# Optimization experiments

Hardware: AMD Instinct MI355X
Metric: run time of the kernel (lower is better)

Reference implementation:

```python
import jax, jax.numpy as jnp
import numpy as np

N_NODES = 50000
N_EDGES = 800000
IN_DIM, HID_DIM, OUT_DIM = 64, 128, 32


def _mpnn_layer(x, src, dst, W, b):
    # message: linear on gathered source features (x_j), then mean-scatter to dst
    msg = x[src] @ W + b                      # [E, out]
    agg = jax.ops.segment_sum(msg, dst, num_segments=N_NODES)
    deg = jax.ops.segment_sum(jnp.ones((msg.shape[0],), msg.dtype), dst,
                              num_segments=N_NODES)
    return agg / jnp.maximum(deg, 1.0)[:, None]  # mean; isolated nodes -> 0


def setup_inputs() -> dict:
    key = jax.random.key(0)
    ks = jax.random.split(key, 8)
    x = jax.random.normal(ks[0], (N_NODES, IN_DIM), dtype=jnp.float32)
    edge_index = jax.random.randint(ks[1], (2, N_EDGES), 0, N_NODES, dtype=jnp.int64)
    W1 = jax.random.normal(ks[2], (IN_DIM, HID_DIM), dtype=jnp.float32) * 0.1
    b1 = jax.random.normal(ks[3], (HID_DIM,), dtype=jnp.float32) * 0.1
    W2 = jax.random.normal(ks[4], (HID_DIM, HID_DIM), dtype=jnp.float32) * 0.1
    b2 = jax.random.normal(ks[5], (HID_DIM,), dtype=jnp.float32) * 0.1
    Wout = jax.random.normal(ks[6], (HID_DIM, OUT_DIM), dtype=jnp.float32) * 0.1
    bout = jax.random.normal(ks[7], (OUT_DIM,), dtype=jnp.float32) * 0.1
    return {"x": x, "edge_index": edge_index, "W1": W1, "b1": b1,
            "W2": W2, "b2": b2, "Wout": Wout, "bout": bout}


def reference(x, edge_index, W1, b1, W2, b2, Wout, bout):
    src, dst = edge_index[0], edge_index[1]  # PyG flow: source_to_target
    h = jax.nn.relu(_mpnn_layer(x, src, dst, W1, b1))
    h = jax.nn.relu(_mpnn_layer(h, src, dst, W2, b2))
    return h @ Wout + bout
```

## Files before the change

### kernel.cpp

```cpp
#include <hip/hip_runtime.h>
#include <hip/hip_bf16.h>

#define N_NODES 50000
#define N_EDGES 800000
#define IN_DIM  64
#define HID_DIM 128
#define OUT_DIM 32
#define ELLW    64

#define NRANGE   8
#define RNG      (N_NODES / NRANGE)
#define ELL_NJ   ((N_EDGES + 255) / 256)

#define CAST_BLKS 3125
#define PW1_BLKS  32
#define PW2_BLKS  64
#define PWO_BLKS  16
#define ZERO_BLKS 49

typedef short bh8_t  __attribute__((ext_vector_type(8)));
typedef float fx4_t  __attribute__((ext_vector_type(4)));

__device__ inline float bflo(unsigned int u) {
    union { unsigned int i; float f; } c; c.i = u << 16; return c.f;
}
__device__ inline float bfhi(unsigned int u) {
    union { unsigned int i; float f; } c; c.i = u & 0xffff0000u; return c.f;
}
__device__ inline unsigned short f2bf(float f) {
    union { float f; unsigned int i; } c; c.f = f;
    unsigned int u = c.i;
    u += 0x7fffu + ((u >> 16) & 1u);
    return (unsigned short)(u >> 16);
}
__device__ inline unsigned int pack2(float a, float b) {
    return (unsigned int)f2bf(a) | ((unsigned int)f2bf(b) << 16);
}
__device__ inline void acc_u4(float* a, uint4 u) {
    a[0] += bflo(u.x); a[1] += bfhi(u.x);
    a[2] += bflo(u.y); a[3] += bfhi(u.y);
    a[4] += bflo(u.z); a[5] += bfhi(u.z);
    a[6] += bflo(u.w); a[7] += bfhi(u.w);
}

template <int K, int M>
__device__ inline void packw_one(const float* __restrict__ W,
                                 unsigned short* __restrict__ Wp, int f) {
    const int k = f / M, m = f % M;
    Wp[((k >> 3) * M + m) * 8 + (k & 7)] = f2bf(W[f]);
}

__global__ void k_prep(const float* __restrict__ x, unsigned short* __restrict__ xb,
                       const float* __restrict__ W1, unsigned short* __restrict__ wp1,
                       const float* __restrict__ W2, unsigned short* __restrict__ wp2,
                       const float* __restrict__ Wout, unsigned short* __restrict__ wpo,
                       int* __restrict__ cnt) {
    const int bid = blockIdx.x;
    if (bid < CAST_BLKS) {
        const int i = bid * 256 + threadIdx.x;
        float4 v = reinterpret_cast<const float4*>(x)[i];
        ushort4 o;
        o.x = f2bf(v.x); o.y = f2bf(v.y); o.z = f2bf(v.z); o.w = f2bf(v.w);
        reinterpret_cast<ushort4*>(xb)[i] = o;
    } else if (bid < CAST_BLKS + PW1_BLKS) {
        packw_one<IN_DIM, HID_DIM>(W1, wp1, (bid - CAST_BLKS) * 256 + threadIdx.x);
    } else if (bid < CAST_BLKS + PW1_BLKS + PW2_BLKS) {
        packw_one<HID_DIM, HID_DIM>(W2, wp2, (bid - CAST_BLKS - PW1_BLKS) * 256 + threadIdx.x);
    } else if (bid < CAST_BLKS + PW1_BLKS + PW2_BLKS + PWO_BLKS) {
        packw_one<HID_DIM, OUT_DIM>(Wout, wpo,
                                    (bid - CAST_BLKS - PW1_BLKS - PW2_BLKS) * 256 + threadIdx.x);
    } else {
        const int zb = bid - (CAST_BLKS + PW1_BLKS + PW2_BLKS + PWO_BLKS);
#pragma unroll
        for (int k2 = 0; k2 < 4; ++k2) {
            const int i = zb * 1024 + k2 * 256 + threadIdx.x;
            if (i < N_NODES) cnt[i] = 0;
        }
    }
}

__global__ __launch_bounds__(256) void k_ell(const int* __restrict__ src,
                                             const int* __restrict__ dst,
                                             int* __restrict__ cnt,
                                             int* __restrict__ ell) {
    const int r  = blockIdx.x & (NRANGE - 1);
    const int j  = blockIdx.x >> 3;
    const int lo = r * RNG;
    const int e  = j * 256 + threadIdx.x;
    const int d  = dst[e];
    if ((unsigned)(d - lo) < (unsigned)RNG) {
        const int p = atomicAdd(&cnt[d], 1);
        if (p < ELLW) ell[(size_t)d * ELLW + p] = src[e];
    }
}

__global__ __launch_bounds__(256) void k_ag1(const unsigned short* __restrict__ xb,
                                             const int* __restrict__ ell,
                                             const int* __restrict__ cnt,
                                             const unsigned short* __restrict__ wp1g,
                                             const float* __restrict__ b1,
                                             unsigned short* __restrict__ h1b) {
    __shared__ unsigned short wp1s[IN_DIM * HID_DIM];
    __shared__ unsigned short m1s[64][72];
    const int tid = threadIdx.x;
#pragma unroll
    for (int f = tid; f < IN_DIM * HID_DIM / 8; f += 256)
        reinterpret_cast<uint4*>(wp1s)[f] = reinterpret_cast<const uint4*>(wp1g)[f];

    const int nloc = tid >> 2, l4 = tid & 3;
    const int node = blockIdx.x * 64 + nloc;
    int c = 0;
    if (node < N_NODES) c = min(cnt[node], ELLW);
    const float inv = (c > 0) ? 1.0f / (float)c : 0.0f;
    const int* er = ell + (size_t)node * ELLW;
    const unsigned short* xbb = xb + l4 * 16;

    float a0[16], a1[16];
#pragma unroll
    for (int v = 0; v < 16; ++v) { a0[v] = 0.f; a1[v] = 0.f; }

    int j = 0;
    for (; j + 4 <= c; j += 4) {
        const int4 e4 = *reinterpret_cast<const int4*>(er + j);
        const unsigned short* r0 = xbb + (size_t)e4.x * IN_DIM;
        const unsigned short* r1 = xbb + (size_t)e4.y * IN_DIM;
        const unsigned short* r2 = xbb + (size_t)e4.z * IN_DIM;
        const unsigned short* r3 = xbb + (size_t)e4.w * IN_DIM;
        uint4 u00 = reinterpret_cast<const uint4*>(r0)[0];
        uint4 u01 = reinterpret_cast<const uint4*>(r0)[1];
        uint4 u10 = reinterpret_cast<const uint4*>(r1)[0];
        uint4 u11 = reinterpret_cast<const uint4*>(r1)[1];
        uint4 u20 = reinterpret_cast<const uint4*>(r2)[0];
        uint4 u21 = reinterpret_cast<const uint4*>(r2)[1];
        uint4 u30 = reinterpret_cast<const uint4*>(r3)[0];
        uint4 u31 = reinterpret_cast<const uint4*>(r3)[1];
        acc_u4(a0, u00); acc_u4(a0 + 8, u01);
        acc_u4(a1, u10); acc_u4(a1 + 8, u11);
        acc_u4(a0, u20); acc_u4(a0 + 8, u21);
        acc_u4(a1, u30); acc_u4(a1 + 8, u31);
    }
    for (; j < c; ++j) {
        const unsigned short* r0 = xbb + (size_t)er[j] * IN_DIM;
        uint4 u00 = reinterpret_cast<const uint4*>(r0)[0];
        uint4 u01 = reinterpret_cast<const uint4*>(r0)[1];
        acc_u4(a0, u00); acc_u4(a0 + 8, u01);
    }

    unsigned int* mw = reinterpret_cast<unsigned int*>(&m1s[nloc][l4 * 16]);
#pragma unroll
    for (int i = 0; i < 8; ++i)
        mw[i] = pack2((a0[2 * i] + a1[2 * i]) * inv,
                      (a0[2 * i + 1] + a1[2 * i + 1]) * inv);
    __syncthreads();

    const int w  = tid >> 6;
    const int l  = tid & 63;
    const int lr = l & 15;
    const int lg = l >> 4;

    fx4_t acc[8];
#pragma unroll
    for (int ct = 0; ct < 8; ++ct) acc[ct] = (fx4_t){0.f, 0.f, 0.f, 0.f};

#pragma unroll
    for (int kc = 0; kc < IN_DIM; kc += 32) {
        const bh8_t af = *reinterpret_cast<const bh8_t*>(&m1s[w * 16 + lr][kc + lg * 8]);
#pragma unroll
        for (int ct = 0; ct < 8; ++ct) {
            const bh8_t bf = *reinterpret_cast<const bh8_t*>(
                &wp1s[(((kc >> 3) + lg) * HID_DIM + ct * 16 + lr) * 8]);
            acc[ct] = __builtin_amdgcn_mfma_f32_16x16x32_bf16(af, bf, acc[ct], 0, 0, 0);
        }
    }

    const int orow0 = blockIdx.x * 64 + w * 16 + lg * 4;
    bool on[4];
#pragma unroll
    for (int r = 0; r < 4; ++r)
        on[r] = (orow0 + r < N_NODES) && (cnt[orow0 + r] > 0);

#pragma unroll
    for (int ct = 0; ct < 8; ++ct) {
        const int m = ct * 16 + lr;
        const float bm = b1[m];
#pragma unroll
        for (int r = 0; r < 4; ++r) {
            const int n = orow0 + r;
            if (n < N_NODES) {
                float v = on[r] ? fmaxf(acc[ct][r] + bm, 0.f) : 0.f;
                h1b[(size_t)n * HID_DIM + m] = f2bf(v);
            }
        }
    }
}

__global__ __launch_bounds__(256) void k_agg2(const unsigned short* __restrict__ Xb,
                                              const int* __restrict__ ell,
                                              const int* __restrict__ cnt,
                                              unsigned short* __restrict__ Mb) {
    const int gid  = threadIdx.x >> 4;
    const int lane = threadIdx.x & 15;
    const int node = blockIdx.x * 16 + gid;
    const int c = min(cnt[node], ELLW);
    const float r = (c > 0) ? 1.0f / (float)c : 0.0f;
    const int* er = ell + (size_t)node * ELLW;
    const unsigned short* base = Xb + lane * 8;

    float a0[8], a1[8];
#pragma unroll
    for (int v = 0; v < 8; ++v) { a0[v] = 0.f; a1[v] = 0.f; }

    int j = 0;
    for (; j + 8 <= c; j += 8) {
        const int4 e03 = *reinterpret_cast<const int4*>(er + j);
        const int4 e47 = *reinterpret_cast<const int4*>(er + j + 4);
        uint4 u0 = *reinterpret_cast<const uint4*>(base + (size_t)e03.x * HID_DIM);
        uint4 u1 = *reinterpret_cast<const uint4*>(base + (size_t)e03.y * HID_DIM);
        uint4 u2 = *reinterpret_cast<const uint4*>(base + (size_t)e03.z * HID_DIM);
        uint4 u3 = *reinterpret_cast<const uint4*>(base + (size_t)e03.w * HID_DIM);
        uint4 u4 = *reinterpret_cast<const uint4*>(base + (size_t)e47.x * HID_DIM);
        uint4 u5 = *reinterpret_cast<const uint4*>(base + (size_t)e47.y * HID_DIM);
        uint4 u6 = *reinterpret_cast<const uint4*>(base + (size_t)e47.z * HID_DIM);
        uint4 u7 = *reinterpret_cast<const uint4*>(base + (size_t)e47.w * HID_DIM);
        acc_u4(a0, u0); acc_u4(a1, u1); acc_u4(a0, u2); acc_u4(a1, u3);
        acc_u4(a0, u4); acc_u4(a1, u5); acc_u4(a0, u6); acc_u4(a1, u7);
    }
    for (; j + 4 <= c; j += 4) {
        const int4 e4 = *reinterpret_cast<const int4*>(er + j);
        uint4 u0 = *reinterpret_cast<const uint4*>(base + (size_t)e4.x * HID_DIM);
        uint4 u1 = *reinterpret_cast<const uint4*>(base + (size_t)e4.y * HID_DIM);
        uint4 u2 = *reinterpret_cast<const uint4*>(base + (size_t)e4.z * HID_DIM);
        uint4 u3 = *reinterpret_cast<const uint4*>(base + (size_t)e4.w * HID_DIM);
        acc_u4(a0, u0); acc_u4(a1, u1); acc_u4(a0, u2); acc_u4(a1, u3);
    }
    for (; j < c; ++j) {
        uint4 u = *reinterpret_cast<const uint4*>(base + (size_t)er[j] * HID_DIM);
        acc_u4(a0, u);
    }

    uint4 o;
    o.x = pack2((a0[0] + a1[0]) * r, (a0[1] + a1[1]) * r);
    o.y = pack2((a0[2] + a1[2]) * r, (a0[3] + a1[3]) * r);
    o.z = pack2((a0[4] + a1[4]) * r, (a0[5] + a1[5]) * r);
    o.w = pack2((a0[6] + a1[6]) * r, (a0[7] + a1[7]) * r);
    *reinterpret_cast<uint4*>(Mb + (size_t)node * HID_DIM + lane * 8) = o;
}

#define H2S (HID_DIM + 8)
__global__ __launch_bounds__(256) void k_mgemm23(const unsigned short* __restrict__ A,
                                                 const unsigned short* __restrict__ Wp2g,
                                                 const unsigned short* __restrict__ Wpog,
                                                 const float* __restrict__ b2,
                                                 const float* __restrict__ bout,
                                                 const int* __restrict__ cnt,
                                                 float* __restrict__ out) {
    __shared__ unsigned short Wp2s[HID_DIM * HID_DIM];
    __shared__ unsigned short Wpos[HID_DIM * OUT_DIM];
    __shared__ unsigned short h2s[64 * H2S];
    const int tid = threadIdx.x;
#pragma unroll
    for (int f = tid; f < HID_DIM * HID_DIM / 8; f += 256)
        reinterpret_cast<uint4*>(Wp2s)[f] = reinterpret_cast<const uint4*>(Wp2g)[f];
#pragma unroll
    for (int f = tid; f < HID_DIM * OUT_DIM / 8; f += 256)
        reinterpret_cast<uint4*>(Wpos)[f] = reinterpret_cast<const uint4*>(Wpog)[f];
    __syncthreads();

    const int w  = tid >> 6;
    const int l  = tid & 63;
    const int lr = l & 15;
    const int lg = l >> 4;
    const int row = blockIdx.x * 64 + w * 16 + lr;
    const bool rok = row < N_NODES;
    const unsigned short* Arow = A + (size_t)row * HID_DIM;

    fx4_t acc[8];
#pragma unroll
    for (int ct = 0; ct < 8; ++ct) acc[ct] = (fx4_t){0.f, 0.f, 0.f, 0.f};

#pragma unroll
    for (int kc = 0; kc < HID_DIM; kc += 32) {
        bh8_t af = {};
        if (rok) af = *reinterpret_cast<const bh8_t*>(Arow + kc + lg * 8);
#pragma unroll
        for (int ct = 0; ct < 8; ++ct) {
            const bh8_t bf = *reinterpret_cast<const bh8_t*>(
                &Wp2s[(((kc >> 3) + lg) * HID_DIM + ct * 16 + lr) * 8]);
            acc[ct] = __builtin_amdgcn_mfma_f32_16x16x32_bf16(af, bf, acc[ct], 0, 0, 0);
        }
    }

    const int lrow0 = w * 16 + lg * 4;
    const int orow0 = blockIdx.x * 64 + lrow0;
    bool on[4];
#pragma unroll
    for (int r = 0; r < 4; ++r)
        on[r] = (orow0 + r < N_NODES) && (cnt[orow0 + r] > 0);

#pragma unroll
    for (int ct = 0; ct < 8; ++ct) {
        const int m = ct * 16 + lr;
        const float bm = b2[m];
#pragma unroll
        for (int r = 0; r < 4; ++r) {
            float v = on[r] ? fmaxf(acc[ct][r] + bm, 0.f) : 0.f;
            h2s[(lrow0 + r) * H2S + m] = f2bf(v);
        }
    }
    __syncthreads();

    fx4_t acc2[2];
#pragma unroll
    for (int ct = 0; ct < 2; ++ct) acc2[ct] = (fx4_t){0.f, 0.f, 0.f, 0.f};

#pragma unroll
    for (int kc = 0; kc < HID_DIM; kc += 32) {
        const bh8_t af = *reinterpret_cast<const bh8_t*>(
            &h2s[(w * 16 + lr) * H2S + kc + lg * 8]);
#pragma unroll
        for (int ct = 0; ct < 2; ++ct) {
            const bh8_t bf = *reinterpret_cast<const bh8_t*>(
                &Wpos[(((kc >> 3) + lg) * OUT_DIM + ct * 16 + lr) * 8]);
            acc2[ct] = __builtin_amdgcn_mfma_f32_16x16x32_bf16(af, bf, acc2[ct], 0, 0, 0);
        }
    }

#pragma unroll
    for (int ct = 0; ct < 2; ++ct) {
        const int m = ct * 16 + lr;
        const float bm = bout[m];
#pragma unroll
        for (int r = 0; r < 4; ++r) {
            const int n = orow0 + r;
            if (n < N_NODES)
                out[(size_t)n * OUT_DIM + m] = acc2[ct][r] + bm;
        }
    }
}

extern "C" void kernel_launch(void* const* d_in, const int* in_sizes, int n_in,
                              void* d_out, int out_size, void* d_ws, size_t ws_size,
                              hipStream_t stream) {
    const float* x    = (const float*)d_in[0];
    const int*   ei   = (const int*)d_in[1];
    const float* W1   = (const float*)d_in[2];
    const float* b1   = (const float*)d_in[3];
    const float* W2   = (const float*)d_in[4];
    const float* b2   = (const float*)d_in[5];
    const float* Wout = (const float*)d_in[6];
    const float* bout = (const float*)d_in[7];
    float* out = (float*)d_out;

    const int* src = ei;
    const int* dst = ei + N_EDGES;

    char* ws = (char*)d_ws;
    int*            cnt = (int*)(ws + 0);
    int*            ell = (int*)(ws + 200000);
    unsigned short* xb  = (unsigned short*)(ws + 13000000);
    unsigned short* h1b = (unsigned short*)(ws + 19400000);
    unsigned short* m2b = (unsigned short*)(ws + 32200000);
    unsigned short* wp1 = (unsigned short*)(ws + 45000000);
    unsigned short* wp2 = (unsigned short*)(ws + 45016384);
    unsigned short* wpo = (unsigned short*)(ws + 45049152);

    const int GB = (N_NODES + 63) / 64;
    const int AB = N_NODES / 16;

    k_prep<<<CAST_BLKS + PW1_BLKS + PW2_BLKS + PWO_BLKS + ZERO_BLKS, 256, 0, stream>>>(
        x, xb, W1, wp1, W2, wp2, Wout, wpo, cnt);
    k_ell<<<ELL_NJ * NRANGE, 256, 0, stream>>>(src, dst, cnt, ell);

    k_ag1<<<GB, 256, 0, stream>>>(xb, ell, cnt, wp1, b1, h1b);

    k_agg2<<<AB, 256, 0, stream>>>(h1b, ell, cnt, m2b);

    k_mgemm23<<<GB, 256, 0, stream>>>(m2b, wp2, wpo, b2, bout, cnt, out);
}
```

Measured before the change: 137.2 us.

## Merge ELL build with prep, split layer-1 aggregation from GEMM, zero counts via memset

Fuses the ELL construction and the cast/weight-pack work into one launch, zeroing the degree counters with hipMemsetAsync beforehand. Layer-1 aggregation moves to a standalone kernel with 16 lanes per node and 8-byte gathers plus deeper unrolling, which writes a bf16 mean buffer. A separate MFMA GEMM kernel then reads that buffer. This aims for more parallel, latency-tolerant gathers and fewer serialized small kernels, at the cost of an extra intermediate round trip through global memory and one more launch.

```diff
diff --git a/kernel.cpp b/kernel.cpp
--- a/kernel.cpp
+++ b/kernel.cpp
@@ -10,13 +10,13 @@
 
 #define NRANGE   8
 #define RNG      (N_NODES / NRANGE)
-#define ELL_NJ   ((N_EDGES + 255) / 256)
+#define ELL_BLKS 25000
 
 #define CAST_BLKS 3125
 #define PW1_BLKS  32
 #define PW2_BLKS  64
 #define PWO_BLKS  16
-#define ZERO_BLKS 49
+#define PREP_BLKS (CAST_BLKS + PW1_BLKS + PW2_BLKS + PWO_BLKS)
 
 typedef short bh8_t  __attribute__((ext_vector_type(8)));
 typedef float fx4_t  __attribute__((ext_vector_type(4)));
@@ -36,6 +36,10 @@
 __device__ inline unsigned int pack2(float a, float b) {
     return (unsigned int)f2bf(a) | ((unsigned int)f2bf(b) << 16);
 }
+__device__ inline void acc_u2(float* a, uint2 u) {
+    a[0] += bflo(u.x); a[1] += bfhi(u.x);
+    a[2] += bflo(u.y); a[3] += bfhi(u.y);
+}
 __device__ inline void acc_u4(float* a, uint4 u) {
     a[0] += bflo(u.x); a[1] += bfhi(u.x);
     a[2] += bflo(u.y); a[3] += bfhi(u.y);
@@ -50,113 +54,117 @@
     Wp[((k >> 3) * M + m) * 8 + (k & 7)] = f2bf(W[f]);
 }
 
-__global__ void k_prep(const float* __restrict__ x, unsigned short* __restrict__ xb,
-                       const float* __restrict__ W1, unsigned short* __restrict__ wp1,
-                       const float* __restrict__ W2, unsigned short* __restrict__ wp2,
-                       const float* __restrict__ Wout, unsigned short* __restrict__ wpo,
-                       int* __restrict__ cnt) {
+__global__ __launch_bounds__(256) void k_pe(const int* __restrict__ src,
+                                            const int* __restrict__ dst,
+                                            int* __restrict__ cnt,
+                                            int* __restrict__ ell,
+                                            const float* __restrict__ x,
+                                            unsigned short* __restrict__ xb,
+                                            const float* __restrict__ W1,
+                                            unsigned short* __restrict__ wp1,
+                                            const float* __restrict__ W2,
+                                            unsigned short* __restrict__ wp2,
+                                            const float* __restrict__ Wout,
+                                            unsigned short* __restrict__ wpo) {
     const int bid = blockIdx.x;
-    if (bid < CAST_BLKS) {
-        const int i = bid * 256 + threadIdx.x;
+    if (bid < ELL_BLKS) {
+        const int r  = bid & (NRANGE - 1);
+        const int j  = bid >> 3;
+        const int lo = r * RNG;
+        const int e  = j * 256 + threadIdx.x;
+        const int d  = dst[e];
+        if ((unsigned)(d - lo) < (unsigned)RNG) {
+            const int p = atomicAdd(&cnt[d], 1);
+            if (p < ELLW) ell[(size_t)d * ELLW + p] = src[e];
+        }
+        return;
+    }
+    const int pb = bid - ELL_BLKS;
+    if (pb < CAST_BLKS) {
+        const int i = pb * 256 + threadIdx.x;
         float4 v = reinterpret_cast<const float4*>(x)[i];
         ushort4 o;
         o.x = f2bf(v.x); o.y = f2bf(v.y); o.z = f2bf(v.z); o.w = f2bf(v.w);
         reinterpret_cast<ushort4*>(xb)[i] = o;
-    } else if (bid < CAST_BLKS + PW1_BLKS) {
-        packw_one<IN_DIM, HID_DIM>(W1, wp1, (bid - CAST_BLKS) * 256 + threadIdx.x);
-    } else if (bid < CAST_BLKS + PW1_BLKS + PW2_BLKS) {
-        packw_one<HID_DIM, HID_DIM>(W2, wp2, (bid - CAST_BLKS - PW1_BLKS) * 256 + threadIdx.x);
-    } else if (bid < CAST_BLKS + PW1_BLKS + PW2_BLKS + PWO_BLKS) {
+    } else if (pb < CAST_BLKS + PW1_BLKS) {
+        packw_one<IN_DIM, HID_DIM>(W1, wp1, (pb - CAST_BLKS) * 256 + threadIdx.x);
+    } else if (pb < CAST_BLKS + PW1_BLKS + PW2_BLKS) {
+        packw_one<HID_DIM, HID_DIM>(W2, wp2, (pb - CAST_BLKS - PW1_BLKS) * 256 + threadIdx.x);
+    } else {
         packw_one<HID_DIM, OUT_DIM>(Wout, wpo,
-                                    (bid - CAST_BLKS - PW1_BLKS - PW2_BLKS) * 256 + threadIdx.x);
-    } else {
-        const int zb = bid - (CAST_BLKS + PW1_BLKS + PW2_BLKS + PWO_BLKS);
-#pragma unroll
-        for (int k2 = 0; k2 < 4; ++k2) {
-            const int i = zb * 1024 + k2 * 256 + threadIdx.x;
-            if (i < N_NODES) cnt[i] = 0;
-        }
-    }
-}
-
-__global__ __launch_bounds__(256) void k_ell(const int* __restrict__ src,
-                                             const int* __restrict__ dst,
-                                             int* __restrict__ cnt,
-                                             int* __restrict__ ell) {
-    const int r  = blockIdx.x & (NRANGE - 1);
-    const int j  = blockIdx.x >> 3;
-    const int lo = r * RNG;
-    const int e  = j * 256 + threadIdx.x;
-    const int d  = dst[e];
-    if ((unsigned)(d - lo) < (unsigned)RNG) {
-        const int p = atomicAdd(&cnt[d], 1);
-        if (p < ELLW) ell[(size_t)d * ELLW + p] = src[e];
-    }
-}
-
-__global__ __launch_bounds__(256) void k_ag1(const unsigned short* __restrict__ xb,
-                                             const int* __restrict__ ell,
-                                             const int* __restrict__ cnt,
-                                             const unsigned short* __restrict__ wp1g,
-                                             const float* __restrict__ b1,
-                                             unsigned short* __restrict__ h1b) {
-    __shared__ unsigned short wp1s[IN_DIM * HID_DIM];
-    __shared__ unsigned short m1s[64][72];
-    const int tid = threadIdx.x;
-#pragma unroll
-    for (int f = tid; f < IN_DIM * HID_DIM / 8; f += 256)
-        reinterpret_cast<uint4*>(wp1s)[f] = reinterpret_cast<const uint4*>(wp1g)[f];
-
-    const int nloc = tid >> 2, l4 = tid & 3;
-    const int node = blockIdx.x * 64 + nloc;
-    int c = 0;
-    if (node < N_NODES) c = min(cnt[node], ELLW);
-    const float inv = (c > 0) ? 1.0f / (float)c : 0.0f;
+                                    (pb - CAST_BLKS - PW1_BLKS - PW2_BLKS) * 256 + threadIdx.x);
+    }
+}
+
+__global__ __launch_bounds__(256) void k_agg1(const unsigned short* __restrict__ Xb,
+                                              const int* __restrict__ ell,
+                                              const int* __restrict__ cnt,
+                                              unsigned short* __restrict__ Mb) {
+    const int gid  = threadIdx.x >> 4;
+    const int lane = threadIdx.x & 15;
+    const int node = blockIdx.x * 16 + gid;
+    const int c = min(cnt[node], ELLW);
+    const float r = (c > 0) ? 1.0f / (float)c : 0.0f;
     const int* er = ell + (size_t)node * ELLW;
-    const unsigned short* xbb = xb + l4 * 16;
-
-    float a0[16], a1[16];
-#pragma unroll
-    for (int v = 0; v < 16; ++v) { a0[v] = 0.f; a1[v] = 0.f; }
+    const unsigned short* base = Xb + lane * 4;
+
+    float a0[4], a1[4];
+#pragma unroll
+    for (int v = 0; v < 4; ++v) { a0[v] = 0.f; a1[v] = 0.f; }
 
     int j = 0;
+    for (; j + 8 <= c; j += 8) {
+        const int4 e03 = *reinterpret_cast<const int4*>(er + j);
+        const int4 e47 = *reinterpret_cast<const int4*>(er + j + 4);
+        uint2 u0 = *reinterpret_cast<const uint2*>(base + (size_t)e03.x * IN_DIM);
+        uint2 u1 = *reinterpret_cast<const uint2*>(base + (size_t)e03.y * IN_DIM);
+        uint2 u2 = *reinterpret_cast<const uint2*>(base + (size_t)e03.z * IN_DIM);
+        uint2 u3 = *reinterpret_cast<const uint2*>(base + (size_t)e03.w * IN_DIM);
+        uint2 u4 = *reinterpret_cast<const uint2*>(base + (size_t)e47.x * IN_DIM);
+        uint2 u5 = *reinterpret_cast<const uint2*>(base + (size_t)e47.y * IN_DIM);
+        uint2 u6 = *reinterpret_cast<const uint2*>(base + (size_t)e47.z * IN_DIM);
+        uint2 u7 = *reinterpret_cast<const uint2*>(base + (size_t)e47.w * IN_DIM);
+        acc_u2(a0, u0); acc_u2(a1, u1); acc_u2(a0, u2); acc_u2(a1, u3);
+        acc_u2(a0, u4); acc_u2(a1, u5); acc_u2(a0, u6); acc_u2(a1, u7);
+    }
     for (; j + 4 <= c; j += 4) {
         const int4 e4 = *reinterpret_cast<const int4*>(er + j);
-        const unsigned short* r0 = xbb + (size_t)e4.x * IN_DIM;
-        const unsigned short* r1 = xbb + (size_t)e4.y * IN_DIM;
-        const unsigned short* r2 = xbb + (size_t)e4.z * IN_DIM;
-        const unsigned short* r3 = xbb + (size_t)e4.w * IN_DIM;
-        uint4 u00 = reinterpret_cast<const uint4*>(r0)[0];
-        uint4 u01 = reinterpret_cast<const uint4*>(r0)[1];
-        uint4 u10 = reinterpret_cast<const uint4*>(r1)[0];
-        uint4 u11 = reinterpret_cast<const uint4*>(r1)[1];
-        uint4 u20 = reinterpret_cast<const uint4*>(r2)[0];
-        uint4 u21 = reinterpret_cast<const uint4*>(r2)[1];
-        uint4 u30 = reinterpret_cast<const uint4*>(r3)[0];
-        uint4 u31 = reinterpret_cast<const uint4*>(r3)[1];
-        acc_u4(a0, u00); acc_u4(a0 + 8, u01);
-        acc_u4(a1, u10); acc_u4(a1 + 8, u11);
-        acc_u4(a0, u20); acc_u4(a0 + 8, u21);
-        acc_u4(a1, u30); acc_u4(a1 + 8, u31);
+        uint2 u0 = *reinterpret_cast<const uint2*>(base + (size_t)e4.x * IN_DIM);
+        uint2 u1 = *reinterpret_cast<const uint2*>(base + (size_t)e4.y * IN_DIM);
+        uint2 u2 = *reinterpret_cast<const uint2*>(base + (size_t)e4.z * IN_DIM);
+        uint2 u3 = *reinterpret_cast<const uint2*>(base + (size_t)e4.w * IN_DIM);
+        acc_u2(a0, u0); acc_u2(a1, u1); acc_u2(a0, u2); acc_u2(a1, u3);
     }
     for (; j < c; ++j) {
-        const unsigned short* r0 = xbb + (size_t)er[j] * IN_DIM;
-        uint4 u00 = reinterpret_cast<const uint4*>(r0)[0];
-        uint4 u01 = reinterpret_cast<const uint4*>(r0)[1];
-        acc_u4(a0, u00); acc_u4(a0 + 8, u01);
-    }
-
-    unsigned int* mw = reinterpret_cast<unsigned int*>(&m1s[nloc][l4 * 16]);
-#pragma unroll
-    for (int i = 0; i < 8; ++i)
-        mw[i] = pack2((a0[2 * i] + a1[2 * i]) * inv,
-                      (a0[2 * i + 1] + a1[2 * i + 1]) * inv);
+        uint2 u = *reinterpret_cast<const uint2*>(base + (size_t)er[j] * IN_DIM);
+        acc_u2(a0, u);
+    }
+
+    uint2 o;
+    o.x = pack2((a0[0] + a1[0]) * r, (a0[1] + a1[1]) * r);
+    o.y = pack2((a0[2] + a1[2]) * r, (a0[3] + a1[3]) * r);
+    *reinterpret_cast<uint2*>(Mb + (size_t)node * IN_DIM + lane * 4) = o;
+}
+
+__global__ __launch_bounds__(256) void k_mgemm1(const unsigned short* __restrict__ A,
+                                                const unsigned short* __restrict__ Wpg,
+                                                const float* __restrict__ b1,
+                                                const int* __restrict__ cnt,
+                                                unsigned short* __restrict__ h1b) {
+    __shared__ unsigned short Wp[IN_DIM * HID_DIM];
+    const int tid = threadIdx.x;
+#pragma unroll
+    for (int f = tid; f < IN_DIM * HID_DIM / 8; f += 256)
+        reinterpret_cast<uint4*>(Wp)[f] = reinterpret_cast<const uint4*>(Wpg)[f];
     __syncthreads();
 
     const int w  = tid >> 6;
     const int l  = tid & 63;
     const int lr = l & 15;
     const int lg = l >> 4;
+    const int row = blockIdx.x * 64 + w * 16 + lr;
+    const bool rok = row < N_NODES;
+    const unsigned short* Arow = A + (size_t)row * IN_DIM;
 
     fx4_t acc[8];
 #pragma unroll
@@ -164,11 +172,12 @@
 
 #pragma unroll
     for (int kc = 0; kc < IN_DIM; kc += 32) {
-        const bh8_t af = *reinterpret_cast<const bh8_t*>(&m1s[w * 16 + lr][kc + lg * 8]);
+        bh8_t af = {};
+        if (rok) af = *reinterpret_cast<const bh8_t*>(Arow + kc + lg * 8);
 #pragma unroll
         for (int ct = 0; ct < 8; ++ct) {
             const bh8_t bf = *reinterpret_cast<const bh8_t*>(
-                &wp1s[(((kc >> 3) + lg) * HID_DIM + ct * 16 + lr) * 8]);
+                &Wp[(((kc >> 3) + lg) * HID_DIM + ct * 16 + lr) * 8]);
             acc[ct] = __builtin_amdgcn_mfma_f32_16x16x32_bf16(af, bf, acc[ct], 0, 0, 0);
         }
     }
@@ -360,18 +369,21 @@
     unsigned short* xb  = (unsigned short*)(ws + 13000000);
     unsigned short* h1b = (unsigned short*)(ws + 19400000);
     unsigned short* m2b = (unsigned short*)(ws + 32200000);
-    unsigned short* wp1 = (unsigned short*)(ws + 45000000);
-    unsigned short* wp2 = (unsigned short*)(ws + 45016384);
-    unsigned short* wpo = (unsigned short*)(ws + 45049152);
+    unsigned short* m1b = (unsigned short*)(ws + 45000000);
+    unsigned short* wp1 = (unsigned short*)(ws + 51400000);
+    unsigned short* wp2 = (unsigned short*)(ws + 51416384);
+    unsigned short* wpo = (unsigned short*)(ws + 51449152);
 
     const int GB = (N_NODES + 63) / 64;
     const int AB = N_NODES / 16;
 
-    k_prep<<<CAST_BLKS + PW1_BLKS + PW2_BLKS + PWO_BLKS + ZERO_BLKS, 256, 0, stream>>>(
-        x, xb, W1, wp1, W2, wp2, Wout, wpo, cnt);
-    k_ell<<<ELL_NJ * NRANGE, 256, 0, stream>>>(src, dst, cnt, ell);
-
-    k_ag1<<<GB, 256, 0, stream>>>(xb, ell, cnt, wp1, b1, h1b);
+    hipMemsetAsync(cnt, 0, N_NODES * sizeof(int), stream);
+
+    k_pe<<<ELL_BLKS + PREP_BLKS, 256, 0, stream>>>(src, dst, cnt, ell,
+                                                   x, xb, W1, wp1, W2, wp2, Wout, wpo);
+
+    k_agg1<<<AB, 256, 0, stream>>>(xb, ell, cnt, m1b);
+    k_mgemm1<<<GB, 256, 0, stream>>>(m1b, wp1, b1, cnt, h1b);
 
     k_agg2<<<AB, 256, 0, stream>>>(h1b, ell, cnt, m2b);
 
```

After: 131.9 us. -3.9%, faster.
